# Kernel optimization log

Hardware: AMD Instinct MI355X
Metric: run time of the kernel (lower is better)

The kernel has to match this reference:

```python
import jax, jax.numpy as jnp
import numpy as np

NPAD = 40  # absorbing-layer padding, from pad(x, 40, 2) in the torch source


def _damp_profile(n, npad):
    # Cerjan-style exponential sponge taper on both edges of a 1-D axis
    i = jnp.arange(n, dtype=jnp.float32)
    left = jnp.where(i < npad, jnp.exp(-(0.015 * (npad - i)) ** 2), 1.0)
    right = jnp.where(i >= n - npad, jnp.exp(-(0.015 * (i - (n - npad - 1))) ** 2), 1.0)
    return (left * right).astype(jnp.float32)


def setup_inputs() -> dict:
    key = jax.random.key(0)
    k1, k2 = jax.random.split(key, 2)
    nz, nx, nt = 26, 120, 1500
    nzp, nxp = nz + 2 * NPAD, nx + 2 * NPAD
    # realistic elastic model: vp 2.5-4 km/s, vs = vp/sqrt(3), rho ~ 2-2.3 g/cc
    vp = 2500.0 + 1500.0 * jax.random.uniform(k1, (nz, nx), dtype=jnp.float32)
    vs = vp / 1.7320508
    den = 2000.0 + 300.0 * jax.random.uniform(k2, (nzp, nxp), dtype=jnp.float32)
    dz, dx, dt = 10.0, 10.0, 1.0e-3
    input_vector = jnp.array([dz, dx, dt, dt / dx], dtype=jnp.float32)
    # Ricker wavelet source
    f0 = 15.0
    t = jnp.arange(nt, dtype=jnp.float32) * dt
    arg = (jnp.pi * f0 * (t - 1.2 / f0)) ** 2
    s = ((1.0 - 2.0 * arg) * jnp.exp(-arg)).astype(jnp.float32)
    temp = jnp.zeros((5, nzp, nxp), dtype=jnp.float32)  # vx, vz, txx, tzz, txz
    return {"vp": vp, "vs": vs, "den": den, "input_vector": input_vector,
            "temp": temp, "s": s, "nt": nt, "isz": NPAD + 2, "isx": NPAD + 60}


def _forward(vp, vs, den, input_vector, temp, s, nt, isz, isx):
    nzp, nxp = den.shape
    nx_int = nxp - 2 * NPAD
    # --- elastic parameter prep (matches torch forward) ---
    vp1 = jnp.pad(vp, NPAD, mode="edge")
    vs1 = jnp.pad(vs, NPAD, mode="edge")
    ca = vp1 ** 2 * den          # lambda + 2*mu
    cm = vs1 ** 2 * den          # mu
    cl = ca - 2.0 * cm           # lambda
    dt = input_vector[2]
    dtx = input_vector[3]
    b = dtx / den                # buoyancy * dt/dx (cm1 = cm, b1 = b are aliases)

    # staggered-grid difference operators (2nd order, Virieux scheme)
    dxp = lambda a: jnp.roll(a, -1, 1) - a
    dxm = lambda a: a - jnp.roll(a, 1, 1)
    dzp = lambda a: jnp.roll(a, -1, 0) - a
    dzm = lambda a: a - jnp.roll(a, 1, 0)

    damp = _damp_profile(nzp, NPAD)[:, None] * _damp_profile(nxp, NPAD)[None, :]

    vx0, vz0, txx0, tzz0, txz0 = temp
    illum0 = jnp.zeros((nzp, nxp), dtype=jnp.float32)

    rec_row = NPAD + 1  # receiver line just below the absorbing top layer

    def step(carry, src):
        vx, vz, txx, tzz, txz, illum = carry
        # velocity update
        vx = (vx + b * (dxp(txx) + dzm(txz))) * damp
        vz = (vz + b * (dzp(tzz) + dxm(txz))) * damp
        exx = dxm(vx)
        ezz = dzm(vz)
        divv = exx + ezz
        # stress update
        txx = (txx + dtx * (ca * exx + cl * ezz)) * damp
        tzz = (tzz + dtx * (cl * exx + ca * ezz)) * damp
        txz = (txz + dtx * cm * (dzp(vx) + dxp(vz))) * damp
        # explosive source injection into normal stresses
        txx = txx.at[isz, isx].add(src * dt)
        tzz = tzz.at[isz, isx].add(src * dt)
        illum = illum + divv * divv
        rec = vz[rec_row, NPAD:NPAD + nx_int]
        return (vx, vz, txx, tzz, txz, illum), rec

    carry0 = (vx0, vz0, txx0, tzz0, txz0, illum0)
    (vx, vz, txx, tzz, txz, illum), seismo_v_d = jax.lax.scan(step, carry0, s[:nt])
    uu1 = jnp.stack([vx, vz, txx, tzz, txz])  # final wavefield state
    return uu1, seismo_v_d, illum


def reference(vp, vs, den, input_vector, temp, s, nt, isz, isx):
    return _forward(vp, vs, den, input_vector, temp, s, nt, isz, isx)
```

## Files before the change

### kernel.cpp

```cpp
#include <hip/hip_runtime.h>

#define NPADC 40
#define NZ 26
#define NXI 120
#define NZP 106
#define NXP 200
#define NCELL (NZP * NXP)

#define KSTEPS 5
#define HALO (2 * KSTEPS)
#define NZB 10
#define NXB 20
#define NBLOCKS (NZB * NXB)
#define TXB 10
#define EXT_XM (TXB + 2 * HALO)
#define EZMAX (11 + 2 * HALO)
#define LDSN (EZMAX * EXT_XM)
#define NTHREADS 1024
#define FLAGSTRIDE 32

#define AGENT __HIP_MEMORY_SCOPE_AGENT

__device__ __forceinline__ float aload(float* p) {
    return __hip_atomic_load(p, __ATOMIC_RELAXED, AGENT);
}
__device__ __forceinline__ void astore(float* p, float v) {
    __hip_atomic_store(p, v, __ATOMIC_RELAXED, AGENT);
}

__device__ __forceinline__ float dprof(int idx, int n) {
#pragma clang fp contract(off)
    float fi = (float)idx;
    float left = 1.0f, right = 1.0f;
    if (idx < NPADC) {
        float a = 0.015f * ((float)NPADC - fi);
        left = expf(-(a * a));
    }
    if (idx >= n - NPADC) {
        float a = 0.015f * (fi - (float)(n - NPADC - 1));
        right = expf(-(a * a));
    }
    return left * right;
}

__global__ void setup_kernel(const float* __restrict__ vp,
                             const float* __restrict__ vs,
                             const float* __restrict__ den,
                             const float* __restrict__ ivec,
                             const float* __restrict__ temp,
                             float* __restrict__ coeff,
                             float* __restrict__ buf0,
                             unsigned* __restrict__ flags) {
#pragma clang fp contract(off)
    int i = blockIdx.x * blockDim.x + threadIdx.x;
    if (i < NBLOCKS * FLAGSTRIDE) flags[i] = 0u;
    if (i >= NCELL) return;
    int z = i / NXP;
    int x = i - z * NXP;

    float dtx = ivec[3];

    int zi = z - NPADC; zi = zi < 0 ? 0 : (zi > NZ - 1 ? NZ - 1 : zi);
    int xi = x - NPADC; xi = xi < 0 ? 0 : (xi > NXI - 1 ? NXI - 1 : xi);
    float vpv = vp[zi * NXI + xi];
    float vsv = vs[zi * NXI + xi];
    float d = den[i];

    float cav = (vpv * vpv) * d;
    float cmv = (vsv * vsv) * d;
    coeff[0 * NCELL + i] = dtx / d;
    coeff[1 * NCELL + i] = dprof(z, NZP) * dprof(x, NXP);
    coeff[2 * NCELL + i] = cav;
    coeff[3 * NCELL + i] = cav - 2.0f * cmv;
    coeff[4 * NCELL + i] = dtx * cmv;

    for (int f = 0; f < 5; ++f)
        buf0[f * NCELL + i] = temp[f * NCELL + i];
}

__global__ __launch_bounds__(NTHREADS)
void persist_kernel(const float* __restrict__ coeff,
                    float* __restrict__ buf0, float* __restrict__ buf1,
                    const float* __restrict__ ivec, const float* __restrict__ s,
                    const int* __restrict__ iszp, const int* __restrict__ isxp,
                    float* __restrict__ fields_out,
                    float* __restrict__ illum_out,
                    float* __restrict__ seismo,
                    unsigned* __restrict__ flags,
                    int nt) {
#pragma clang fp contract(off)
    __shared__ float lds[5][LDSN];

    const int tid = threadIdx.x;
    const int bid = blockIdx.x;
    const int zb = bid / NXB, xb = bid - zb * NXB;
    const int z0  = (zb < 6) ? 11 * zb : 66 + (zb - 6) * 10;
    const int tzb = (zb < 6) ? 11 : 10;
    const int x0  = xb * TXB;
    const int ez  = tzb + 2 * HALO;
    const int ncl = ez * EXT_XM;
    const float dt  = ivec[2];
    const float dtx = ivec[3];
    const int isz = *iszp, isx = *isxp;

    const int rc = tid;
    const bool valid = rc < ncl;
    int izv = -1000, ixv = -1000, g = 0, seis = -1;
    bool inter = false;
    float cb = 0.f, cd = 0.f, cca = 0.f, ccl = 0.f, cdtcm = 0.f;
    if (valid) {
        int iz = rc / EXT_XM, ix = rc - iz * EXT_XM;
        izv = iz; ixv = ix;
        int gz = z0 - HALO + iz; gz += (gz < 0) ? NZP : 0; gz -= (gz >= NZP) ? NZP : 0;
        int gx = x0 - HALO + ix; gx += (gx < 0) ? NXP : 0; gx -= (gx >= NXP) ? NXP : 0;
        g = gz * NXP + gx;
        cb    = coeff[0 * NCELL + g];
        cd    = coeff[1 * NCELL + g];
        cca   = coeff[2 * NCELL + g];
        ccl   = coeff[3 * NCELL + g];
        cdtcm = coeff[4 * NCELL + g];
        int liz = iz - HALO, lix = ix - HALO;
        inter = (liz >= 0 && liz < tzb && lix >= 0 && lix < TXB);
        int gzi = z0 + liz, gxi = x0 + lix;
        seis = (inter && gzi == NPADC + 1 && gxi >= NPADC && gxi < NPADC + NXI)
                   ? (gxi - NPADC) : -1;
    }
    int lzs = isz - (z0 - HALO); lzs = ((lzs % NZP) + NZP) % NZP;
    int lxs = isx - (x0 - HALO); lxs = ((lxs % NXP) + NXP) % NXP;
    const int src_rc = (lzs < ez && lxs < EXT_XM) ? lzs * EXT_XM + lxs : -1;

    int nbflag = -1;
    if (tid < 8) {
        int idx = (tid < 4) ? tid : tid + 1;
        int dz = idx / 3 - 1, dx = idx % 3 - 1;
        int nzb = zb + dz; nzb += (nzb < 0) ? NZB : 0; nzb -= (nzb >= NZB) ? NZB : 0;
        int nxb = xb + dx; nxb += (nxb < 0) ? NXB : 0; nxb -= (nxb >= NXB) ? NXB : 0;
        nbflag = (nzb * NXB + nxb) * FLAGSTRIDE;
    }

    float ilacc = 0.0f;
    float rvx = 0.f, rvz = 0.f, rtxx = 0.f, rtzz = 0.f, rtxz = 0.f;

    int t0 = 0, parity = 0;
    unsigned chunk = 0;
    while (t0 < nt) {
        const int ks = (nt - t0 >= KSTEPS) ? KSTEPS : (nt - t0);
        const bool last = (t0 + ks >= nt);
        float* srcb = parity ? buf1 : buf0;
        float* dstb = last ? fields_out : (parity ? buf0 : buf1);

        if (valid && (chunk == 0 || !inter)) {
            rvx  = aload(&srcb[0 * NCELL + g]);
            rvz  = aload(&srcb[1 * NCELL + g]);
            rtxx = aload(&srcb[2 * NCELL + g]);
            rtzz = aload(&srcb[3 * NCELL + g]);
            rtxz = aload(&srcb[4 * NCELL + g]);
            lds[0][rc] = rvx;
            lds[1][rc] = rvz;
            lds[2][rc] = rtxx;
            lds[3][rc] = rtzz;
            lds[4][rc] = rtxz;
        }
        __syncthreads();

        for (int k = 1; k <= ks; ++k) {
            const int t = t0 + k - 1;
            {
                const int p = 2 * k - 1;
                if (izv >= p && izv < ez - p && ixv >= p && ixv < EXT_XM - p) {
                    float txx_p1 = lds[2][rc + 1];
                    float tzz_pE = lds[3][rc + EXT_XM];
                    float txz_mE = lds[4][rc - EXT_XM];
                    float txz_m1 = lds[4][rc - 1];
                    float t1 = txx_p1 - rtxx;
                    float t2 = rtxz - txz_mE;
                    float nvx = (rvx + cb * (t1 + t2)) * cd;
                    float t3 = tzz_pE - rtzz;
                    float t4 = rtxz - txz_m1;
                    float nvz = (rvz + cb * (t3 + t4)) * cd;
                    rvx = nvx; rvz = nvz;
                    lds[0][rc] = nvx;
                    lds[1][rc] = nvz;
                    if (seis >= 0) seismo[t * NXI + seis] = nvz;
                }
            }
            __syncthreads();
            {
                const int p = 2 * k;
                if (izv >= p && izv < ez - p && ixv >= p && ixv < EXT_XM - p) {
                    float vx_m1 = lds[0][rc - 1];
                    float vz_mE = lds[1][rc - EXT_XM];
                    float vx_pE = lds[0][rc + EXT_XM];
                    float vz_p1 = lds[1][rc + 1];
                    float exx = rvx - vx_m1;
                    float ezz = rvz - vz_mE;
                    float e1 = cca * exx;
                    float e2 = ccl * ezz;
                    float ntxx = (rtxx + dtx * (e1 + e2)) * cd;
                    float e3 = ccl * exx;
                    float e4 = cca * ezz;
                    float ntzz = (rtzz + dtx * (e3 + e4)) * cd;
                    float p1 = vx_pE - rvx;
                    float p2 = vz_p1 - rvz;
                    float ntxz = (rtxz + cdtcm * (p1 + p2)) * cd;
                    if (rc == src_rc) {
                        float sv = s[t] * dt;
                        ntxx += sv;
                        ntzz += sv;
                    }
                    rtxx = ntxx; rtzz = ntzz; rtxz = ntxz;
                    lds[2][rc] = ntxx;
                    lds[3][rc] = ntzz;
                    lds[4][rc] = ntxz;
                    if (inter) {
                        float divv = exx + ezz;
                        ilacc += divv * divv;
                    }
                }
            }
            if (k < ks) __syncthreads();
        }

        if (inter) {
            astore(&dstb[0 * NCELL + g], rvx);
            astore(&dstb[1 * NCELL + g], rvz);
            astore(&dstb[2 * NCELL + g], rtxx);
            astore(&dstb[3 * NCELL + g], rtzz);
            astore(&dstb[4 * NCELL + g], rtxz);
            if (last) illum_out[g] = ilacc;
        }

        t0 += ks; parity ^= 1; ++chunk;

        if (!last) {
            asm volatile("s_waitcnt vmcnt(0)" ::: "memory");
            __syncthreads();
            if (tid == 0)
                __hip_atomic_store(&flags[bid * FLAGSTRIDE], chunk,
                                   __ATOMIC_RELAXED, AGENT);
            if (tid < 8) {
                while (__hip_atomic_load(&flags[nbflag], __ATOMIC_RELAXED, AGENT)
                       < chunk)
                    __builtin_amdgcn_s_sleep(1);
            }
            __syncthreads();
        }
    }
}

extern "C" void kernel_launch(void* const* d_in, const int* in_sizes, int n_in,
                              void* d_out, int out_size, void* d_ws, size_t ws_size,
                              hipStream_t stream) {
    const float* vp   = (const float*)d_in[0];
    const float* vs   = (const float*)d_in[1];
    const float* den  = (const float*)d_in[2];
    const float* ivec = (const float*)d_in[3];
    const float* temp = (const float*)d_in[4];
    const float* s    = (const float*)d_in[5];
    const int*   isz  = (const int*)d_in[7];
    const int*   isx  = (const int*)d_in[8];
    int nt = in_sizes[5];

    float* out    = (float*)d_out;
    float* fields = out;
    float* seismo = out + 5 * NCELL;
    float* illum  = seismo + (size_t)nt * NXI;

    float* ws    = (float*)d_ws;
    float* coeff = ws;
    float* buf0  = ws + 5 * NCELL;
    float* buf1  = ws + 10 * NCELL;
    unsigned* flags = (unsigned*)(ws + 15 * NCELL);

    setup_kernel<<<(NCELL + 255) / 256, 256, 0, stream>>>(
        vp, vs, den, ivec, temp, coeff, buf0, flags);

    persist_kernel<<<NBLOCKS, NTHREADS, 0, stream>>>(
        coeff, buf0, buf1, ivec, s, isz, isx,
        fields, illum, seismo, flags, nt);
}
```

Before: 1.302 ms.

## Interleave halo exchange buffers per cell and overlap neighbor flag polling

Changes the global ping-pong exchange buffers from a field-major layout to a per-cell interleaved layout with a stride of 8 floats. Each cell's five fields are now moved with two 64-bit atomics plus one 32-bit atomic instead of five 32-bit atomics. Neighbor-flag polling moves to threads in the last wavefront and is attempted once per inner step during compute, so the barrier wait at chunk end can often be skipped. This aims to cut memory transactions and synchronization latency between blocks, at the cost of a larger workspace and more scattered access to each field.

```diff
diff --git a/kernel.cpp b/kernel.cpp
--- a/kernel.cpp
+++ b/kernel.cpp
@@ -18,14 +18,29 @@
 #define LDSN (EZMAX * EXT_XM)
 #define NTHREADS 1024
 #define FLAGSTRIDE 32
+#define CST 8
 
 #define AGENT __HIP_MEMORY_SCOPE_AGENT
 
-__device__ __forceinline__ float aload(float* p) {
-    return __hip_atomic_load(p, __ATOMIC_RELAXED, AGENT);
-}
-__device__ __forceinline__ void astore(float* p, float v) {
+__device__ __forceinline__ unsigned long long ald64(const float* p) {
+    return __hip_atomic_load((unsigned long long*)p, __ATOMIC_RELAXED, AGENT);
+}
+__device__ __forceinline__ float ald32(const float* p) {
+    return __hip_atomic_load((float*)p, __ATOMIC_RELAXED, AGENT);
+}
+__device__ __forceinline__ void ast64(float* p, float lo, float hi) {
+    unsigned long long u = (unsigned long long)__float_as_uint(lo)
+                         | ((unsigned long long)__float_as_uint(hi) << 32);
+    __hip_atomic_store((unsigned long long*)p, u, __ATOMIC_RELAXED, AGENT);
+}
+__device__ __forceinline__ void ast32(float* p, float v) {
     __hip_atomic_store(p, v, __ATOMIC_RELAXED, AGENT);
+}
+__device__ __forceinline__ float u64lo(unsigned long long u) {
+    return __uint_as_float((unsigned)(u & 0xffffffffull));
+}
+__device__ __forceinline__ float u64hi(unsigned long long u) {
+    return __uint_as_float((unsigned)(u >> 32));
 }
 
 __device__ __forceinline__ float dprof(int idx, int n) {
@@ -49,7 +64,7 @@
                              const float* __restrict__ ivec,
                              const float* __restrict__ temp,
                              float* __restrict__ coeff,
-                             float* __restrict__ buf0,
+                             float* __restrict__ bufA,
                              unsigned* __restrict__ flags) {
 #pragma clang fp contract(off)
     int i = blockIdx.x * blockDim.x + threadIdx.x;
@@ -74,13 +89,14 @@
     coeff[3 * NCELL + i] = cav - 2.0f * cmv;
     coeff[4 * NCELL + i] = dtx * cmv;
 
+    float* cell = bufA + (size_t)i * CST;
     for (int f = 0; f < 5; ++f)
-        buf0[f * NCELL + i] = temp[f * NCELL + i];
+        cell[f] = temp[f * NCELL + i];
 }
 
 __global__ __launch_bounds__(NTHREADS)
 void persist_kernel(const float* __restrict__ coeff,
-                    float* __restrict__ buf0, float* __restrict__ buf1,
+                    float* __restrict__ bufA, float* __restrict__ bufB,
                     const float* __restrict__ ivec, const float* __restrict__ s,
                     const int* __restrict__ iszp, const int* __restrict__ isxp,
                     float* __restrict__ fields_out,
@@ -129,9 +145,10 @@
     int lxs = isx - (x0 - HALO); lxs = ((lxs % NXP) + NXP) % NXP;
     const int src_rc = (lzs < ez && lxs < EXT_XM) ? lzs * EXT_XM + lxs : -1;
 
-    int nbflag = -1;
-    if (tid < 8) {
-        int idx = (tid < 4) ? tid : tid + 1;
+    const int pi = tid - 960;
+    int nbflag = 0;
+    if (pi >= 0 && pi < 8) {
+        int idx = (pi < 4) ? pi : pi + 1;
         int dz = idx / 3 - 1, dx = idx % 3 - 1;
         int nzb = zb + dz; nzb += (nzb < 0) ? NZB : 0; nzb -= (nzb >= NZB) ? NZB : 0;
         int nxb = xb + dx; nxb += (nxb < 0) ? NXB : 0; nxb -= (nxb >= NXB) ? NXB : 0;
@@ -146,15 +163,19 @@
     while (t0 < nt) {
         const int ks = (nt - t0 >= KSTEPS) ? KSTEPS : (nt - t0);
         const bool last = (t0 + ks >= nt);
-        float* srcb = parity ? buf1 : buf0;
-        float* dstb = last ? fields_out : (parity ? buf0 : buf1);
+        const unsigned tgt = chunk + 1;
+        float* srcb = parity ? bufB : bufA;
+        float* dstb = parity ? bufA : bufB;
+        bool pseen = false;
 
         if (valid && (chunk == 0 || !inter)) {
-            rvx  = aload(&srcb[0 * NCELL + g]);
-            rvz  = aload(&srcb[1 * NCELL + g]);
-            rtxx = aload(&srcb[2 * NCELL + g]);
-            rtzz = aload(&srcb[3 * NCELL + g]);
-            rtxz = aload(&srcb[4 * NCELL + g]);
+            const float* cp = srcb + (size_t)g * CST;
+            unsigned long long u0 = ald64(cp);
+            unsigned long long u1 = ald64(cp + 2);
+            float f4 = ald32(cp + 4);
+            rvx  = u64lo(u0); rvz  = u64hi(u0);
+            rtxx = u64lo(u1); rtzz = u64hi(u1);
+            rtxz = f4;
             lds[0][rc] = rvx;
             lds[1][rc] = rvz;
             lds[2][rc] = rtxx;
@@ -165,6 +186,8 @@
 
         for (int k = 1; k <= ks; ++k) {
             const int t = t0 + k - 1;
+            if (!last && !pseen && pi >= 0 && pi < 8)
+                pseen = (__hip_atomic_load(&flags[nbflag], __ATOMIC_RELAXED, AGENT) >= tgt);
             {
                 const int p = 2 * k - 1;
                 if (izv >= p && izv < ez - p && ixv >= p && ixv < EXT_XM - p) {
@@ -222,12 +245,19 @@
         }
 
         if (inter) {
-            astore(&dstb[0 * NCELL + g], rvx);
-            astore(&dstb[1 * NCELL + g], rvz);
-            astore(&dstb[2 * NCELL + g], rtxx);
-            astore(&dstb[3 * NCELL + g], rtzz);
-            astore(&dstb[4 * NCELL + g], rtxz);
-            if (last) illum_out[g] = ilacc;
+            if (!last) {
+                float* dp = dstb + (size_t)g * CST;
+                ast64(dp, rvx, rvz);
+                ast64(dp + 2, rtxx, rtzz);
+                ast32(dp + 4, rtxz);
+            } else {
+                fields_out[0 * NCELL + g] = rvx;
+                fields_out[1 * NCELL + g] = rvz;
+                fields_out[2 * NCELL + g] = rtxx;
+                fields_out[3 * NCELL + g] = rtzz;
+                fields_out[4 * NCELL + g] = rtxz;
+                illum_out[g] = ilacc;
+            }
         }
 
         t0 += ks; parity ^= 1; ++chunk;
@@ -238,10 +268,12 @@
             if (tid == 0)
                 __hip_atomic_store(&flags[bid * FLAGSTRIDE], chunk,
                                    __ATOMIC_RELAXED, AGENT);
-            if (tid < 8) {
-                while (__hip_atomic_load(&flags[nbflag], __ATOMIC_RELAXED, AGENT)
-                       < chunk)
-                    __builtin_amdgcn_s_sleep(1);
+            if (pi >= 0 && pi < 8) {
+                while (!pseen) {
+                    pseen = (__hip_atomic_load(&flags[nbflag], __ATOMIC_RELAXED,
+                                               AGENT) >= tgt);
+                    if (!pseen) __builtin_amdgcn_s_sleep(1);
+                }
             }
             __syncthreads();
         }
@@ -268,14 +300,14 @@
 
     float* ws    = (float*)d_ws;
     float* coeff = ws;
-    float* buf0  = ws + 5 * NCELL;
-    float* buf1  = ws + 10 * NCELL;
-    unsigned* flags = (unsigned*)(ws + 15 * NCELL);
+    float* bufA  = ws + 5 * NCELL;
+    float* bufB  = ws + 13 * NCELL;
+    unsigned* flags = (unsigned*)(ws + 21 * NCELL);
 
     setup_kernel<<<(NCELL + 255) / 256, 256, 0, stream>>>(
-        vp, vs, den, ivec, temp, coeff, buf0, flags);
+        vp, vs, den, ivec, temp, coeff, bufA, flags);
 
     persist_kernel<<<NBLOCKS, NTHREADS, 0, stream>>>(
-        coeff, buf0, buf1, ivec, s, isz, isx,
+        coeff, bufA, bufB, ivec, s, isz, isx,
         fields, illum, seismo, flags, nt);
 }
```

Result: slower. 1.540 ms (+18.3%).
